# Performance work log

Hardware: AMD Instinct MI355X
Metric: run time of the kernel (lower is better)

Reference implementation:

```python
import jax, jax.numpy as jnp
import numpy as np

TOKENS, HIDDEN = 2048, 1024
N_EXPERTS, INTER, TOPK = 8, 2816, 2
RENORMALIZE = True


def setup_inputs() -> dict:
    key = jax.random.key(0)
    k1, k2, k3, k4 = jax.random.split(key, 4)
    x = jax.random.normal(k1, (TOKENS, HIDDEN), dtype=jnp.float32)
    gating_output = jax.random.normal(k2, (TOKENS, N_EXPERTS), dtype=jnp.float32)
    # stacked gate_proj+up_proj per expert: [E, 2*I, H]
    w1 = jax.random.normal(k3, (N_EXPERTS, 2 * INTER, HIDDEN), dtype=jnp.float32) * 0.02
    # down_proj per expert: [E, H, I]
    w2 = jax.random.normal(k4, (N_EXPERTS, HIDDEN, INTER), dtype=jnp.float32) * 0.02
    return {"x": x, "gating_output": gating_output, "w1": w1, "w2": w2}


def _moe(x, gating_output, w1, w2):
    # fused_topk: softmax over router logits, then top-k, then renormalize
    probs = jax.nn.softmax(gating_output, axis=-1)              # [T, E]
    topk_w, topk_ids = jax.lax.top_k(probs, TOPK)                # [T, K]
    if RENORMALIZE:
        topk_w = topk_w / jnp.sum(topk_w, axis=-1, keepdims=True)
    # fused_experts: gate/up proj -> SiLU(gate)*up -> down proj, per expert
    h = jnp.einsum('th,eih->tei', x, w1)                         # [T, E, 2I]
    gate, up = h[..., :INTER], h[..., INTER:]
    act = jax.nn.silu(gate) * up                                 # [T, E, I]
    out_e = jnp.einsum('tei,ehi->teh', act, w2)                  # [T, E, H]
    # combine: gather selected experts and weight them
    sel = jnp.take_along_axis(out_e, topk_ids[:, :, None], axis=1)  # [T, K, H]
    return jnp.sum(sel * topk_w[:, :, None].astype(sel.dtype), axis=1)  # [T, H]


def reference(x, gating_output, w1, w2):
    return _moe(x, gating_output, w1, w2)
```

## Files before the change

kernel.cpp:

```cpp
#include <hip/hip_runtime.h>
#include <hip/hip_bf16.h>

#define TOKENS 2048
#define HIDDEN 1024
#define NEXP   8
#define INTER  2816
#define N1     5632
#define ROWCAP 5120
#define MT     40
#define NT1    44
#define NT2    8
#define SPLITK 2
#define CONVB  2048

typedef __attribute__((ext_vector_type(8))) short short8;
typedef __attribute__((ext_vector_type(4))) float f32x4;

typedef unsigned int __attribute__((address_space(1))) as1_uint;
typedef unsigned int __attribute__((address_space(3))) as3_uint;

__device__ __forceinline__ void gload16(const void* g, void* l) {
  __builtin_amdgcn_global_load_lds((const as1_uint*)g, (as3_uint*)l, 16, 0, 0);
}

__device__ __forceinline__ unsigned short f2bf(float f) {
  unsigned u = __float_as_uint(f);
  u += 0x7fff + ((u >> 16) & 1);
  return (unsigned short)(u >> 16);
}
__device__ __forceinline__ float bf2f(unsigned short h) {
  return __uint_as_float(((unsigned)h) << 16);
}
__device__ __forceinline__ unsigned short bfs(float x) {
  __hip_bfloat16 h = __float2bfloat16(x);
  return *reinterpret_cast<unsigned short*>(&h);
}
__device__ __forceinline__ short8 pack8(f32x4 lo, f32x4 hi) {
  short8 o;
  o[0] = (short)bfs(lo[0]); o[1] = (short)bfs(lo[1]); o[2] = (short)bfs(lo[2]); o[3] = (short)bfs(lo[3]);
  o[4] = (short)bfs(hi[0]); o[5] = (short)bfs(hi[1]); o[6] = (short)bfs(hi[2]); o[7] = (short)bfs(hi[3]);
  return o;
}

__global__ void k_routing(const float* __restrict__ gate, int* __restrict__ ctrl,
                          int* __restrict__ tkid, float* __restrict__ tkw) {
  int t = blockIdx.x * blockDim.x + threadIdx.x;
  if (t >= TOKENS) return;
  float l[8];
#pragma unroll
  for (int i = 0; i < 8; i++) l[i] = gate[t * 8 + i];
  int i0 = 0; float m0 = l[0];
#pragma unroll
  for (int i = 1; i < 8; i++) if (l[i] > m0) { m0 = l[i]; i0 = i; }
  int i1 = -1; float m1 = -3.4e38f;
#pragma unroll
  for (int i = 0; i < 8; i++) if (i != i0 && l[i] > m1) { m1 = l[i]; i1 = i; }
  float e  = __expf(m1 - m0);
  float w0 = 1.f / (1.f + e);
  float w1 = e / (1.f + e);
  tkid[2 * t] = i0; tkid[2 * t + 1] = i1;
  tkw[2 * t] = w0;  tkw[2 * t + 1] = w1;
  atomicAdd(&ctrl[i0], 1);
  atomicAdd(&ctrl[i1], 1);
}

__global__ void k_base(int* ctrl) {
  if (threadIdx.x == 0) {
    int a = 0;
    for (int e = 0; e < 8; e++) { ctrl[16 + e] = a; a += ((ctrl[e] + 127) >> 7) << 7; }
  }
}

__global__ void k_fill(int* __restrict__ ctrl, const int* __restrict__ tkid,
                       int* __restrict__ rtok, int* __restrict__ trow) {
  int t = blockIdx.x * blockDim.x + threadIdx.x;
  if (t >= TOKENS) return;
#pragma unroll
  for (int k = 0; k < 2; k++) {
    int e = tkid[2 * t + k];
    int pos = atomicAdd(&ctrl[8 + e], 1);
    int row = ctrl[16 + e] + pos;
    rtok[row] = t;
    trow[2 * t + k] = row;
  }
}

__global__ void k_prep(const float* __restrict__ x, const int* __restrict__ ctrl,
                       const int* __restrict__ rtok, unsigned short* __restrict__ Abf,
                       const float* __restrict__ w2, unsigned short* __restrict__ w2b) {
  int b = blockIdx.x;
  if (b < ROWCAP) {
    int row = b;
    int e = -1, local = 0;
    for (int i = 0; i < 8; i++) {
      int bb = ctrl[16 + i], p = ((ctrl[i] + 127) >> 7) << 7;
      if (row >= bb && row < bb + p) { e = i; local = row - bb; break; }
    }
    if (e < 0) return;
    int tid = threadIdx.x;
    unsigned short* dst = Abf + (size_t)row * HIDDEN;
    if (local < ctrl[e]) {
      int t = rtok[row];
      float4 v = ((const float4*)(x + (size_t)t * HIDDEN))[tid];
      ushort4 o; o.x = f2bf(v.x); o.y = f2bf(v.y); o.z = f2bf(v.z); o.w = f2bf(v.w);
      ((ushort4*)dst)[tid] = o;
    } else {
      ushort4 z; z.x = 0; z.y = 0; z.z = 0; z.w = 0;
      ((ushort4*)dst)[tid] = z;
    }
  } else {
    const int n8 = NEXP * HIDDEN * INTER / 8;
    int i = (b - ROWCAP) * blockDim.x + threadIdx.x;
    int stride = CONVB * blockDim.x;
    for (; i < n8; i += stride) {
      float4 a = ((const float4*)w2)[2 * i];
      float4 c = ((const float4*)w2)[2 * i + 1];
      union { ushort us[8]; uint4 v; } o;
      o.us[0] = f2bf(a.x); o.us[1] = f2bf(a.y); o.us[2] = f2bf(a.z); o.us[3] = f2bf(a.w);
      o.us[4] = f2bf(c.x); o.us[5] = f2bf(c.y); o.us[6] = f2bf(c.z); o.us[7] = f2bf(c.w);
      ((uint4*)w2b)[i] = o.v;
    }
  }
}

__device__ __forceinline__ int tile_lookup(const int* ctrl, int mt, int* ml) {
  int a0 = 0;
  for (int i = 0; i < 8; i++) {
    int pt = (ctrl[i] + 127) >> 7;
    if (mt < a0 + pt) { *ml = mt - a0; return i; }
    a0 += pt;
  }
  return -1;
}

__global__ __launch_bounds__(256, 3) void k_gemm1(const float* __restrict__ w1,
    const unsigned short* __restrict__ Abf, unsigned short* __restrict__ act,
    const int* __restrict__ ctrl) {
  union __align__(16) LdsU {
    struct { unsigned char A[16384]; unsigned char Bf[32768]; } st;
    unsigned short hb[128 * 132];
  };
  __shared__ LdsU lds;
  int bid = blockIdx.x;
  int wg = (bid & 7) * (NT1 * MT / 8) + (bid >> 3);
  int nt = wg / MT, mt = wg % MT;
  int ml; int e = tile_lookup(ctrl, mt, &ml);
  if (e < 0) return;
  int tid = threadIdx.x, lane = tid & 63, wid = tid >> 6, wr = wid >> 1, wc = wid & 1;
  int rbase = ctrl[16 + e] + ml * 128;
  const unsigned char* Ab = (const unsigned char*)(Abf + (size_t)rbase * HIDDEN);
  const unsigned char* Bw = (const unsigned char*)(w1 + (size_t)e * N1 * HIDDEN);
  int l3 = lane >> 3, l4 = lane >> 4, l15 = lane & 15;
  int swzA = ((lane & 7) ^ l3) << 4;

  unsigned aoff[4], boff[8];
#pragma unroll
  for (int i = 0; i < 4; i++) {
    int g = wid * 4 + i;
    aoff[i] = (unsigned)(g * 8 + l3) * (HIDDEN * 2) + swzA;
  }
#pragma unroll
  for (int i = 0; i < 8; i++) {
    int r = (wid * 8 + i) * 4 + l4;
    int grow = (r < 64) ? nt * 64 + r : INTER + nt * 64 + (r - 64);
    boff[i] = (unsigned)grow * (HIDDEN * 4) + ((l15 ^ (r & 15)) << 4);
  }

  f32x4 acc[4][4];
  f32x4 zero = {0.f, 0.f, 0.f, 0.f};
#pragma unroll
  for (int i = 0; i < 4; i++)
#pragma unroll
    for (int j = 0; j < 4; j++) acc[i][j] = zero;

  for (int kk = 0; kk < HIDDEN / 64; ++kk) {
#pragma unroll
    for (int i = 0; i < 4; i++)
      gload16(Ab + (size_t)aoff[i] + kk * 128, &lds.st.A[(wid * 4 + i) * 1024]);
#pragma unroll
    for (int i = 0; i < 8; i++)
      gload16(Bw + (size_t)boff[i] + kk * 256, &lds.st.Bf[(wid * 8 + i) * 1024]);
    __syncthreads();
#pragma unroll
    for (int ks = 0; ks < 2; ++ks) {
      short8 a[4], b[4];
#pragma unroll
      for (int mi = 0; mi < 4; mi++) {
        int row = wr * 64 + mi * 16 + l15;
        int koff = ks * 64 + (l4 << 4);
        a[mi] = *(const short8*)&lds.st.A[row * 128 + (koff ^ ((row & 7) << 4))];
      }
#pragma unroll
      for (int ni = 0; ni < 4; ni++) {
        int r = wc * 64 + ni * 16 + l15;
        int c = ks * 8 + l4 * 2;
        f32x4 lo = *(const f32x4*)&lds.st.Bf[r * 256 + ((c ^ (r & 15)) << 4)];
        f32x4 hi = *(const f32x4*)&lds.st.Bf[r * 256 + (((c + 1) ^ (r & 15)) << 4)];
        b[ni] = pack8(lo, hi);
      }
#pragma unroll
      for (int mi = 0; mi < 4; mi++)
#pragma unroll
        for (int ni = 0; ni < 4; ni++)
          acc[mi][ni] = __builtin_amdgcn_mfma_f32_16x16x32_bf16(a[mi], b[ni], acc[mi][ni], 0, 0, 0);
    }
    __syncthreads();
  }
#pragma unroll
  for (int mi = 0; mi < 4; mi++)
#pragma unroll
    for (int ni = 0; ni < 4; ni++)
#pragma unroll
      for (int r = 0; r < 4; r++) {
        int row = wr * 64 + mi * 16 + (l4 << 2) + r;
        int col = wc * 64 + ni * 16 + l15;
        lds.hb[row * 132 + col] = f2bf(acc[mi][ni][r]);
      }
  __syncthreads();
  {
    int r = tid >> 1, ch = (tid & 1) * 32;
    unsigned short* orow = act + (size_t)(rbase + r) * INTER + nt * 64 + ch;
    const unsigned short* hrow = &lds.hb[r * 132];
#pragma unroll
    for (int j = 0; j < 32; j += 4) {
      ushort4 o;
#pragma unroll
      for (int q = 0; q < 4; q++) {
        float g = bf2f(hrow[ch + j + q]);
        float u = bf2f(hrow[64 + ch + j + q]);
        float s = g / (1.f + __expf(-g));
        ((unsigned short*)&o)[q] = f2bf(s * u);
      }
      *(ushort4*)(orow + j) = o;
    }
  }
}

__global__ __launch_bounds__(256, 4) void k_gemm2b(const unsigned short* __restrict__ w2b,
    const unsigned short* __restrict__ act, float* __restrict__ Pb,
    const int* __restrict__ ctrl) {
  struct __align__(16) Lds2 { unsigned char A[16384]; unsigned char B[16384]; };
  __shared__ Lds2 lds;
  int bid = blockIdx.x;
  int wg = (bid & 7) * (NT2 * MT * SPLITK / 8) + (bid >> 3);
  int mt = wg % MT;
  int p = wg / MT;
  int z = p & 1, nt = p >> 1;
  int ml; int e = tile_lookup(ctrl, mt, &ml);
  if (e < 0) return;
  int tid = threadIdx.x, lane = tid & 63, wid = tid >> 6, wr = wid >> 1, wc = wid & 1;
  int rbase = ctrl[16 + e] + ml * 128;
  const int KST = (INTER / 64) / SPLITK;
  const unsigned char* Ab = (const unsigned char*)(act + (size_t)rbase * INTER) + (size_t)z * KST * 128;
  const unsigned char* Bb = (const unsigned char*)(w2b + (size_t)e * HIDDEN * INTER) + (size_t)z * KST * 128;
  int l3 = lane >> 3, l4 = lane >> 4, l15 = lane & 15;
  int swz = ((lane & 7) ^ l3) << 4;

  unsigned aoff[4], boff[4];
#pragma unroll
  for (int i = 0; i < 4; i++) {
    int g = wid * 4 + i;
    aoff[i] = (unsigned)(g * 8 + l3) * (INTER * 2) + swz;
    boff[i] = (unsigned)(nt * 128 + g * 8 + l3) * (INTER * 2) + swz;
  }

  f32x4 acc[4][4];
  f32x4 zero = {0.f, 0.f, 0.f, 0.f};
#pragma unroll
  for (int i = 0; i < 4; i++)
#pragma unroll
    for (int j = 0; j < 4; j++) acc[i][j] = zero;

  for (int kk = 0; kk < KST; ++kk) {
#pragma unroll
    for (int i = 0; i < 4; i++)
      gload16(Ab + (size_t)aoff[i] + kk * 128, &lds.A[(wid * 4 + i) * 1024]);
#pragma unroll
    for (int i = 0; i < 4; i++)
      gload16(Bb + (size_t)boff[i] + kk * 128, &lds.B[(wid * 4 + i) * 1024]);
    __syncthreads();
#pragma unroll
    for (int ks = 0; ks < 2; ++ks) {
      short8 a[4], b[4];
#pragma unroll
      for (int mi = 0; mi < 4; mi++) {
        int row = wr * 64 + mi * 16 + l15;
        int koff = ks * 64 + (l4 << 4);
        a[mi] = *(const short8*)&lds.A[row * 128 + (koff ^ ((row & 7) << 4))];
      }
#pragma unroll
      for (int ni = 0; ni < 4; ni++) {
        int row = wc * 64 + ni * 16 + l15;
        int koff = ks * 64 + (l4 << 4);
        b[ni] = *(const short8*)&lds.B[row * 128 + (koff ^ ((row & 7) << 4))];
      }
#pragma unroll
      for (int mi = 0; mi < 4; mi++)
#pragma unroll
        for (int ni = 0; ni < 4; ni++)
          acc[mi][ni] = __builtin_amdgcn_mfma_f32_16x16x32_bf16(a[mi], b[ni], acc[mi][ni], 0, 0, 0);
    }
    __syncthreads();
  }
  float* P = Pb + (size_t)z * ROWCAP * HIDDEN;
#pragma unroll
  for (int mi = 0; mi < 4; mi++)
#pragma unroll
    for (int ni = 0; ni < 4; ni++) {
      int col = nt * 128 + wc * 64 + ni * 16 + l15;
#pragma unroll
      for (int r = 0; r < 4; r++) {
        int row = rbase + wr * 64 + mi * 16 + (l4 << 2) + r;
        P[(size_t)row * HIDDEN + col] = acc[mi][ni][r];
      }
    }
}

__global__ void k_finish(const float* __restrict__ Pb,
                         const int* __restrict__ trow, const float* __restrict__ tkw,
                         float* __restrict__ out) {
  int t = blockIdx.x, c = threadIdx.x;
  const float* P0 = Pb;
  const float* P1 = Pb + (size_t)ROWCAP * HIDDEN;
  int r0 = trow[2 * t], r1 = trow[2 * t + 1];
  float w0 = tkw[2 * t], w1 = tkw[2 * t + 1];
  float4 a0 = ((const float4*)(P0 + (size_t)r0 * HIDDEN))[c];
  float4 b0 = ((const float4*)(P1 + (size_t)r0 * HIDDEN))[c];
  float4 a1 = ((const float4*)(P0 + (size_t)r1 * HIDDEN))[c];
  float4 b1 = ((const float4*)(P1 + (size_t)r1 * HIDDEN))[c];
  float4 o;
  o.x = w0 * (a0.x + b0.x) + w1 * (a1.x + b1.x);
  o.y = w0 * (a0.y + b0.y) + w1 * (a1.y + b1.y);
  o.z = w0 * (a0.z + b0.z) + w1 * (a1.z + b1.z);
  o.w = w0 * (a0.w + b0.w) + w1 * (a1.w + b1.w);
  ((float4*)(out + (size_t)t * HIDDEN))[c] = o;
}

extern "C" void kernel_launch(void* const* d_in, const int* in_sizes, int n_in,
                              void* d_out, int out_size, void* d_ws, size_t ws_size,
                              hipStream_t stream) {
  const float* x      = (const float*)d_in[0];
  const float* gating = (const float*)d_in[1];
  const float* w1     = (const float*)d_in[2];
  const float* w2     = (const float*)d_in[3];
  float* out = (float*)d_out;
  char* ws = (char*)d_ws;

  int*   ctrl = (int*)ws;
  int*   tkid = (int*)(ws + 4096);
  float* tkw  = (float*)(ws + 24576);
  int*   rtok = (int*)(ws + 45056);
  int*   trow = (int*)(ws + 73728);
  size_t off_Abf = 131072;
  size_t off_act = off_Abf + (size_t)ROWCAP * HIDDEN * 2;
  size_t off_w2b = off_act + (size_t)ROWCAP * INTER * 2;
  size_t off_P   = off_w2b + (size_t)NEXP * HIDDEN * INTER * 2;
  unsigned short* Abf  = (unsigned short*)(ws + off_Abf);
  unsigned short* actb = (unsigned short*)(ws + off_act);
  unsigned short* w2b  = (unsigned short*)(ws + off_w2b);
  float* Pb = (float*)(ws + off_P);

  hipMemsetAsync(ws, 0, 1024, stream);

  k_routing<<<TOKENS / 256, 256, 0, stream>>>(gating, ctrl, tkid, tkw);
  k_base<<<1, 64, 0, stream>>>(ctrl);
  k_fill<<<TOKENS / 256, 256, 0, stream>>>(ctrl, tkid, rtok, trow);
  k_prep<<<ROWCAP + CONVB, 256, 0, stream>>>(x, ctrl, rtok, Abf, w2, w2b);
  k_gemm1<<<NT1 * MT, 256, 0, stream>>>(w1, Abf, actb, ctrl);
  k_gemm2b<<<NT2 * MT * SPLITK, 256, 0, stream>>>(w2b, actb, Pb, ctrl);
  k_finish<<<TOKENS, 256, 0, stream>>>(Pb, trow, tkw, out);
}
```

Before: 246.4 us.

## Halve gemm1 K-tile, fuse SiLU epilogue in registers, split-K 4, drop k_base

gemm1 now stages a K=32 slice per iteration, which halves its LDS footprint and raises the occupancy target to 6 blocks. Gate and up columns are interleaved per wave so SiLU*up is computed straight from the accumulators, removing the LDS round-trip epilogue. gemm2 moves from split-K 2 to split-K 4, and k_finish sums all partials, which adds partial-buffer traffic in exchange for more parallel blocks. The k_base launch is removed and expert bases are recomputed inline. The risks are more barriers per K step and uncoalesced scalar bf16 stores in the new epilogue.

```diff
diff --git a/kernel.cpp b/kernel.cpp
--- a/kernel.cpp
+++ b/kernel.cpp
@@ -10,7 +10,7 @@
 #define MT     40
 #define NT1    44
 #define NT2    8
-#define SPLITK 2
+#define SPLITK 4
 #define CONVB  2048
 
 typedef __attribute__((ext_vector_type(8))) short short8;
@@ -64,11 +64,10 @@
   atomicAdd(&ctrl[i1], 1);
 }
 
-__global__ void k_base(int* ctrl) {
-  if (threadIdx.x == 0) {
-    int a = 0;
-    for (int e = 0; e < 8; e++) { ctrl[16 + e] = a; a += ((ctrl[e] + 127) >> 7) << 7; }
-  }
+__device__ __forceinline__ int base_of(const int* __restrict__ cnt, int e) {
+  int a = 0;
+  for (int i = 0; i < e; i++) a += ((cnt[i] + 127) >> 7) << 7;
+  return a;
 }
 
 __global__ void k_fill(int* __restrict__ ctrl, const int* __restrict__ tkid,
@@ -79,7 +78,7 @@
   for (int k = 0; k < 2; k++) {
     int e = tkid[2 * t + k];
     int pos = atomicAdd(&ctrl[8 + e], 1);
-    int row = ctrl[16 + e] + pos;
+    int row = base_of(ctrl, e) + pos;
     rtok[row] = t;
     trow[2 * t + k] = row;
   }
@@ -91,10 +90,11 @@
   int b = blockIdx.x;
   if (b < ROWCAP) {
     int row = b;
-    int e = -1, local = 0;
+    int e = -1, local = 0, b0 = 0;
     for (int i = 0; i < 8; i++) {
-      int bb = ctrl[16 + i], p = ((ctrl[i] + 127) >> 7) << 7;
-      if (row >= bb && row < bb + p) { e = i; local = row - bb; break; }
+      int p = ((ctrl[i] + 127) >> 7) << 7;
+      if (row >= b0 && row < b0 + p) { e = i; local = row - b0; break; }
+      b0 += p;
     }
     if (e < 0) return;
     int tid = threadIdx.x;
@@ -123,47 +123,49 @@
   }
 }
 
-__device__ __forceinline__ int tile_lookup(const int* ctrl, int mt, int* ml) {
-  int a0 = 0;
+__device__ __forceinline__ int tile_lookup2(const int* ctrl, int mt, int* ml, int* rb) {
+  int a0 = 0, b0 = 0;
   for (int i = 0; i < 8; i++) {
     int pt = (ctrl[i] + 127) >> 7;
-    if (mt < a0 + pt) { *ml = mt - a0; return i; }
-    a0 += pt;
+    if (mt < a0 + pt) { *ml = mt - a0; *rb = b0; return i; }
+    a0 += pt; b0 += pt << 7;
   }
   return -1;
 }
 
-__global__ __launch_bounds__(256, 3) void k_gemm1(const float* __restrict__ w1,
+__global__ __launch_bounds__(256, 6) void k_gemm1(const float* __restrict__ w1,
     const unsigned short* __restrict__ Abf, unsigned short* __restrict__ act,
     const int* __restrict__ ctrl) {
-  union __align__(16) LdsU {
-    struct { unsigned char A[16384]; unsigned char Bf[32768]; } st;
-    unsigned short hb[128 * 132];
-  };
-  __shared__ LdsU lds;
+  struct __align__(16) Lds1 { unsigned char A[8192]; unsigned char Bf[16384]; };
+  __shared__ Lds1 lds;
   int bid = blockIdx.x;
   int wg = (bid & 7) * (NT1 * MT / 8) + (bid >> 3);
   int nt = wg / MT, mt = wg % MT;
-  int ml; int e = tile_lookup(ctrl, mt, &ml);
+  int ml, rb; int e = tile_lookup2(ctrl, mt, &ml, &rb);
   if (e < 0) return;
   int tid = threadIdx.x, lane = tid & 63, wid = tid >> 6, wr = wid >> 1, wc = wid & 1;
-  int rbase = ctrl[16 + e] + ml * 128;
+  int rbase = rb + ml * 128;
   const unsigned char* Ab = (const unsigned char*)(Abf + (size_t)rbase * HIDDEN);
   const unsigned char* Bw = (const unsigned char*)(w1 + (size_t)e * N1 * HIDDEN);
-  int l3 = lane >> 3, l4 = lane >> 4, l15 = lane & 15;
-  int swzA = ((lane & 7) ^ l3) << 4;
-
-  unsigned aoff[4], boff[8];
+  int l4j = (lane >> 4) & 3, l15 = lane & 15;
+
+  unsigned aoff[2];
+#pragma unroll
+  for (int i = 0; i < 2; i++) {
+    int g = wid * 2 + i;
+    int row = g * 16 + (lane >> 2);
+    int ch = (lane & 3) ^ ((lane >> 3) & 3);
+    aoff[i] = (unsigned)row * (HIDDEN * 2) + (ch << 4);
+  }
+  unsigned boff[4];
 #pragma unroll
   for (int i = 0; i < 4; i++) {
     int g = wid * 4 + i;
-    aoff[i] = (unsigned)(g * 8 + l3) * (HIDDEN * 2) + swzA;
-  }
-#pragma unroll
-  for (int i = 0; i < 8; i++) {
-    int r = (wid * 8 + i) * 4 + l4;
-    int grow = (r < 64) ? nt * 64 + r : INTER + nt * 64 + (r - 64);
-    boff[i] = (unsigned)grow * (HIDDEN * 4) + ((l15 ^ (r & 15)) << 4);
+    int r = g * 8 + (lane >> 3);
+    int wcr = r >> 6, sub = r & 63;
+    int grow = (sub < 32) ? (nt * 64 + wcr * 32 + sub)
+                          : (INTER + nt * 64 + wcr * 32 + (sub - 32));
+    boff[i] = (unsigned)grow * (HIDDEN * 4) + ((((lane & 7) ^ (lane >> 3)) & 7) << 4);
   }
 
   f32x4 acc[4][4];
@@ -173,70 +175,51 @@
 #pragma unroll
     for (int j = 0; j < 4; j++) acc[i][j] = zero;
 
-  for (int kk = 0; kk < HIDDEN / 64; ++kk) {
+  for (int kk = 0; kk < HIDDEN / 32; ++kk) {
+#pragma unroll
+    for (int i = 0; i < 2; i++)
+      gload16(Ab + (size_t)aoff[i] + kk * 64, &lds.A[(wid * 2 + i) * 1024]);
 #pragma unroll
     for (int i = 0; i < 4; i++)
-      gload16(Ab + (size_t)aoff[i] + kk * 128, &lds.st.A[(wid * 4 + i) * 1024]);
-#pragma unroll
-    for (int i = 0; i < 8; i++)
-      gload16(Bw + (size_t)boff[i] + kk * 256, &lds.st.Bf[(wid * 8 + i) * 1024]);
+      gload16(Bw + (size_t)boff[i] + kk * 128, &lds.Bf[(wid * 4 + i) * 1024]);
     __syncthreads();
-#pragma unroll
-    for (int ks = 0; ks < 2; ++ks) {
-      short8 a[4], b[4];
-#pragma unroll
-      for (int mi = 0; mi < 4; mi++) {
-        int row = wr * 64 + mi * 16 + l15;
-        int koff = ks * 64 + (l4 << 4);
-        a[mi] = *(const short8*)&lds.st.A[row * 128 + (koff ^ ((row & 7) << 4))];
+    short8 a[4], b[4];
+#pragma unroll
+    for (int mi = 0; mi < 4; mi++) {
+      int row = wr * 64 + mi * 16 + l15;
+      a[mi] = *(const short8*)&lds.A[row * 64 + ((l4j ^ ((l15 >> 1) & 3)) << 4)];
+    }
+#pragma unroll
+    for (int ni = 0; ni < 4; ni++) {
+      int r = wc * 64 + ni * 16 + l15;
+      int c0 = 2 * l4j;
+      f32x4 lo = *(const f32x4*)&lds.Bf[r * 128 + ((c0 ^ (r & 7)) << 4)];
+      f32x4 hi = *(const f32x4*)&lds.Bf[r * 128 + (((c0 + 1) ^ (r & 7)) << 4)];
+      b[ni] = pack8(lo, hi);
+    }
+#pragma unroll
+    for (int mi = 0; mi < 4; mi++)
+#pragma unroll
+      for (int ni = 0; ni < 4; ni++)
+        acc[mi][ni] = __builtin_amdgcn_mfma_f32_16x16x32_bf16(a[mi], b[ni], acc[mi][ni], 0, 0, 0);
+    __syncthreads();
+  }
+#pragma unroll
+  for (int mi = 0; mi < 4; mi++)
+#pragma unroll
+    for (int ni = 0; ni < 2; ni++) {
+      int col = nt * 64 + wc * 32 + ni * 16 + l15;
+#pragma unroll
+      for (int q = 0; q < 4; q++) {
+        int row = rbase + wr * 64 + mi * 16 + l4j * 4 + q;
+        float g = acc[mi][ni][q], u = acc[mi][ni + 2][q];
+        float s = g / (1.f + __expf(-g));
+        act[(size_t)row * INTER + col] = f2bf(s * u);
       }
-#pragma unroll
-      for (int ni = 0; ni < 4; ni++) {
-        int r = wc * 64 + ni * 16 + l15;
-        int c = ks * 8 + l4 * 2;
-        f32x4 lo = *(const f32x4*)&lds.st.Bf[r * 256 + ((c ^ (r & 15)) << 4)];
-        f32x4 hi = *(const f32x4*)&lds.st.Bf[r * 256 + (((c + 1) ^ (r & 15)) << 4)];
-        b[ni] = pack8(lo, hi);
-      }
-#pragma unroll
-      for (int mi = 0; mi < 4; mi++)
-#pragma unroll
-        for (int ni = 0; ni < 4; ni++)
-          acc[mi][ni] = __builtin_amdgcn_mfma_f32_16x16x32_bf16(a[mi], b[ni], acc[mi][ni], 0, 0, 0);
-    }
-    __syncthreads();
-  }
-#pragma unroll
-  for (int mi = 0; mi < 4; mi++)
-#pragma unroll
-    for (int ni = 0; ni < 4; ni++)
-#pragma unroll
-      for (int r = 0; r < 4; r++) {
-        int row = wr * 64 + mi * 16 + (l4 << 2) + r;
-        int col = wc * 64 + ni * 16 + l15;
-        lds.hb[row * 132 + col] = f2bf(acc[mi][ni][r]);
-      }
-  __syncthreads();
-  {
-    int r = tid >> 1, ch = (tid & 1) * 32;
-    unsigned short* orow = act + (size_t)(rbase + r) * INTER + nt * 64 + ch;
-    const unsigned short* hrow = &lds.hb[r * 132];
-#pragma unroll
-    for (int j = 0; j < 32; j += 4) {
-      ushort4 o;
-#pragma unroll
-      for (int q = 0; q < 4; q++) {
-        float g = bf2f(hrow[ch + j + q]);
-        float u = bf2f(hrow[64 + ch + j + q]);
-        float s = g / (1.f + __expf(-g));
-        ((unsigned short*)&o)[q] = f2bf(s * u);
-      }
-      *(ushort4*)(orow + j) = o;
-    }
-  }
-}
-
-__global__ __launch_bounds__(256, 4) void k_gemm2b(const unsigned short* __restrict__ w2b,
+    }
+}
+
+__global__ __launch_bounds__(256, 5) void k_gemm2b(const unsigned short* __restrict__ w2b,
     const unsigned short* __restrict__ act, float* __restrict__ Pb,
     const int* __restrict__ ctrl) {
   struct __align__(16) Lds2 { unsigned char A[16384]; unsigned char B[16384]; };
@@ -245,11 +228,11 @@
   int wg = (bid & 7) * (NT2 * MT * SPLITK / 8) + (bid >> 3);
   int mt = wg % MT;
   int p = wg / MT;
-  int z = p & 1, nt = p >> 1;
-  int ml; int e = tile_lookup(ctrl, mt, &ml);
+  int z = p & 3, nt = p >> 2;
+  int ml, rb; int e = tile_lookup2(ctrl, mt, &ml, &rb);
   if (e < 0) return;
   int tid = threadIdx.x, lane = tid & 63, wid = tid >> 6, wr = wid >> 1, wc = wid & 1;
-  int rbase = ctrl[16 + e] + ml * 128;
+  int rbase = rb + ml * 128;
   const int KST = (INTER / 64) / SPLITK;
   const unsigned char* Ab = (const unsigned char*)(act + (size_t)rbase * INTER) + (size_t)z * KST * 128;
   const unsigned char* Bb = (const unsigned char*)(w2b + (size_t)e * HIDDEN * INTER) + (size_t)z * KST * 128;
@@ -320,19 +303,22 @@
                          const int* __restrict__ trow, const float* __restrict__ tkw,
                          float* __restrict__ out) {
   int t = blockIdx.x, c = threadIdx.x;
-  const float* P0 = Pb;
-  const float* P1 = Pb + (size_t)ROWCAP * HIDDEN;
   int r0 = trow[2 * t], r1 = trow[2 * t + 1];
   float w0 = tkw[2 * t], w1 = tkw[2 * t + 1];
-  float4 a0 = ((const float4*)(P0 + (size_t)r0 * HIDDEN))[c];
-  float4 b0 = ((const float4*)(P1 + (size_t)r0 * HIDDEN))[c];
-  float4 a1 = ((const float4*)(P0 + (size_t)r1 * HIDDEN))[c];
-  float4 b1 = ((const float4*)(P1 + (size_t)r1 * HIDDEN))[c];
+  float4 s0 = {0.f, 0.f, 0.f, 0.f}, s1 = {0.f, 0.f, 0.f, 0.f};
+#pragma unroll
+  for (int z = 0; z < SPLITK; z++) {
+    const float* P = Pb + (size_t)z * ROWCAP * HIDDEN;
+    float4 a = ((const float4*)(P + (size_t)r0 * HIDDEN))[c];
+    float4 b = ((const float4*)(P + (size_t)r1 * HIDDEN))[c];
+    s0.x += a.x; s0.y += a.y; s0.z += a.z; s0.w += a.w;
+    s1.x += b.x; s1.y += b.y; s1.z += b.z; s1.w += b.w;
+  }
   float4 o;
-  o.x = w0 * (a0.x + b0.x) + w1 * (a1.x + b1.x);
-  o.y = w0 * (a0.y + b0.y) + w1 * (a1.y + b1.y);
-  o.z = w0 * (a0.z + b0.z) + w1 * (a1.z + b1.z);
-  o.w = w0 * (a0.w + b0.w) + w1 * (a1.w + b1.w);
+  o.x = w0 * s0.x + w1 * s1.x;
+  o.y = w0 * s0.y + w1 * s1.y;
+  o.z = w0 * s0.z + w1 * s1.z;
+  o.w = w0 * s0.w + w1 * s1.w;
   ((float4*)(out + (size_t)t * HIDDEN))[c] = o;
 }
 
@@ -363,7 +349,6 @@
   hipMemsetAsync(ws, 0, 1024, stream);
 
   k_routing<<<TOKENS / 256, 256, 0, stream>>>(gating, ctrl, tkid, tkw);
-  k_base<<<1, 64, 0, stream>>>(ctrl);
   k_fill<<<TOKENS / 256, 256, 0, stream>>>(ctrl, tkid, rtok, trow);
   k_prep<<<ROWCAP + CONVB, 256, 0, stream>>>(x, ctrl, rtok, Abf, w2, w2b);
   k_gemm1<<<NT1 * MT, 256, 0, stream>>>(w1, Abf, actb, ctrl);
```

After: 795.6 us. +222.8%, slower.
